# Optimization experiments

Measured on AMD Instinct MI355X. Metric: run time of the kernel, lower is better.

Reference implementation:

```python
import jax, jax.numpy as jnp
import numpy as np

B, P, N, E, H, D = 64, 256, 1000, 128, 8, 16
SQRT_E = 11.313708498984761  # sqrt(embedding_dim)
CLIP = 10.0                  # logit_clipping


def setup_inputs() -> dict:
    key = jax.random.key(0)
    ks = jax.random.split(key, 9)
    s = 0.05  # weight init scale
    return {
        "encoded_nodes": jax.random.normal(ks[0], (B, N, E), jnp.float32),
        "encoded_last_node": jax.random.normal(ks[1], (B, P, E), jnp.float32),
        "attr": jax.random.uniform(ks[2], (B, P, 1), jnp.float32),
        "ninf_mask": jnp.zeros((B, P, N), jnp.float32),
        # params stored [in, out] (apply as x @ W, equals torch Linear with W.T)
        "Wq_last": jax.random.normal(ks[3], (E + 1, H * D), jnp.float32) * s,
        "Wk": jax.random.normal(ks[4], (E, H * D), jnp.float32) * s,
        "Wv": jax.random.normal(ks[5], (E, H * D), jnp.float32) * s,
        "Wo": jax.random.normal(ks[6], (H * D, E), jnp.float32) * s,
        "bo": jax.random.normal(ks[7], (E,), jnp.float32) * s,
    }


def reference(encoded_nodes, encoded_last_node, attr, ninf_mask,
              Wq_last, Wk, Wv, Wo, bo):
    # set_kv: project encoded nodes to per-head K, V  -> [B, N, H, D]
    k = (encoded_nodes @ Wk).reshape(B, N, H, D)
    v = (encoded_nodes @ Wv).reshape(B, N, H, D)

    # query from (last node embedding, attr) -> [B, P, H, D]
    input_cat = jnp.concatenate([encoded_last_node, attr], axis=2)  # [B,P,E+1]
    q = (input_cat @ Wq_last).reshape(B, P, H, D)

    # multi-head attention with additive rank-3 -inf mask
    inv_sqrt_d = 1.0 / jnp.sqrt(jnp.float32(D))
    scores = jnp.einsum("bphd,bnhd->bhpn", q, k) * inv_sqrt_d
    scores = scores + ninf_mask[:, None, :, :]            # [B,H,P,N]
    weights = jax.nn.softmax(scores, axis=-1)
    out = jnp.einsum("bhpn,bnhd->bphd", weights, v).reshape(B, P, H * D)

    mh = out @ Wo + bo                                    # [B,P,E]

    # single-head tanh-clipped scoring against encoded nodes
    score = jnp.einsum("bpe,bne->bpn", mh, encoded_nodes) / SQRT_E
    score_masked = CLIP * jnp.tanh(score) + ninf_mask
    probs = jax.nn.softmax(score_masked, axis=2)          # [B,P,N]
    return probs
```

## Files before the change

### kernel.cpp

```cpp
#include <hip/hip_runtime.h>

#define BB 64
#define PP 256
#define NN 1000
#define NP 1024
#define EE 128
#define HH 8
#define DD 16

typedef __fp16 v4h __attribute__((ext_vector_type(4)));
typedef float v4f __attribute__((ext_vector_type(4)));


__global__ __launch_bounds__(256) void k1_qproj(const float* __restrict__ ln,
                                                const float* __restrict__ attr,
                                                const float* __restrict__ Wq,
                                                __fp16* __restrict__ Qh) {
    __shared__ __fp16 wt[128 * 132];
    __shared__ float attrs[64];
    const int tid = threadIdx.x;
    const int row0 = blockIdx.x * 64;
    for (int i = tid; i < 128 * 128; i += 256) {
        int k = i >> 7, n = i & 127;
        wt[n * 132 + k] = (__fp16)Wq[i];
    }
    if (tid < 64) attrs[tid] = attr[row0 + tid];
    __syncthreads();

    const int wid = tid >> 6, lane = tid & 63;
    const int lp = lane & 15, lg = lane >> 4;
    const int rb = row0 + wid * 16;

    const float* arow = ln + (size_t)(rb + lp) * 128;
    v4f acc[8];
#pragma unroll
    for (int cf = 0; cf < 8; cf++) acc[cf] = (v4f){0.f, 0.f, 0.f, 0.f};

#pragma unroll
    for (int k0 = 0; k0 < 8; k0++) {
        float4 av = *(const float4*)&arow[k0 * 16 + 4 * lg];
        v4h af;
        af[0] = (__fp16)av.x; af[1] = (__fp16)av.y;
        af[2] = (__fp16)av.z; af[3] = (__fp16)av.w;
#pragma unroll
        for (int cf = 0; cf < 8; cf++) {
            v4h bf = *(const v4h*)&wt[(cf * 16 + lp) * 132 + k0 * 16 + 4 * lg];
            acc[cf] = __builtin_amdgcn_mfma_f32_16x16x16f16(af, bf, acc[cf], 0, 0, 0);
        }
    }

#pragma unroll
    for (int cf = 0; cf < 8; cf++) {
        const int col = cf * 16 + lp;
        const float w128 = Wq[128 * 128 + col];
#pragma unroll
        for (int r = 0; r < 4; r++) {
            const int rl = wid * 16 + 4 * lg + r;
            float v = (acc[cf][r] + attrs[rl] * w128) * 0.25f;
            Qh[(size_t)(row0 + rl) * 128 + col] = (__fp16)v;
        }
    }
}

__global__ __launch_bounds__(256) void k2_kv(const float* __restrict__ nodes,
                                             const float* __restrict__ Wk,
                                             const float* __restrict__ Wv,
                                             __fp16* __restrict__ Kf,
                                             __fp16* __restrict__ Vf) {
    __shared__ __fp16 wt[128 * 132];
    const int tid = threadIdx.x;
    const int b = blockIdx.y;
    const int kv = blockIdx.z;
    const float* W = (kv == 0) ? Wk : Wv;
    for (int i = tid; i < 128 * 128; i += 256) {
        int k = i >> 7, n = i & 127;
        wt[n * 132 + k] = (__fp16)W[i];
    }
    __syncthreads();

    const int wid = tid >> 6, lane = tid & 63;
    const int lp = lane & 15, lg = lane >> 4;
    const int nb = blockIdx.x * 64 + wid * 16;

    int nr = nb + lp;
    if (nr >= NN) nr = NN - 1;
    const float* arow = nodes + (size_t)(b * NN + nr) * 128;

    v4f acc[8];
#pragma unroll
    for (int cf = 0; cf < 8; cf++) acc[cf] = (v4f){0.f, 0.f, 0.f, 0.f};

#pragma unroll
    for (int k0 = 0; k0 < 8; k0++) {
        float4 av = *(const float4*)&arow[k0 * 16 + 4 * lg];
        v4h af;
        af[0] = (__fp16)av.x; af[1] = (__fp16)av.y;
        af[2] = (__fp16)av.z; af[3] = (__fp16)av.w;
#pragma unroll
        for (int cf = 0; cf < 8; cf++) {
            v4h bf = *(const v4h*)&wt[(cf * 16 + lp) * 132 + k0 * 16 + 4 * lg];
            acc[cf] = __builtin_amdgcn_mfma_f32_16x16x16f16(af, bf, acc[cf], 0, 0, 0);
        }
    }

    if (kv == 0) {
#pragma unroll
        for (int cf = 0; cf < 8; cf++) {
            const size_t base = ((size_t)(b * HH + cf) << 14) + lp;
#pragma unroll
            for (int r = 0; r < 4; r++) {
                const int n = nb + 4 * lg + r;
                Kf[base + (size_t)n * 16] = (n < NN) ? (__fp16)acc[cf][r] : (__fp16)0.f;
            }
        }
    } else {
#pragma unroll
        for (int cf = 0; cf < 8; cf++) {
            v4h pk;
#pragma unroll
            for (int r = 0; r < 4; r++) {
                const int n = nb + 4 * lg + r;
                pk[r] = (n < NN) ? (__fp16)acc[cf][r] : (__fp16)0.f;
            }
            *(v4h*)&Vf[(((size_t)(b * HH + cf) * 16 + lp) << 10) + nb + 4 * lg] = pk;
        }
    }
}

__global__ __launch_bounds__(256) void k3_attn(const __fp16* __restrict__ Qh,
                                               const __fp16* __restrict__ Kf,
                                               const __fp16* __restrict__ Vf,
                                               const float* __restrict__ mask,
                                               float* __restrict__ Aout) {
    const int tid = threadIdx.x;
    const int bid = blockIdx.x;
    const int b = bid & 63;
    const int c = bid >> 6;
    const int hg = c & 3, pt = c >> 2;
    const int h0 = hg * 2;
    const int p0 = pt * 64;

    const int wid = tid >> 6, lane = tid & 63;
    const int lp = lane & 15, lg = lane >> 4;
    const int pw = p0 + wid * 16;

    v4h qf[2];
    {
        const __fp16* qrow = Qh + (size_t)(b * PP + pw + lp) * 128 + h0 * 16 + 4 * lg;
#pragma unroll
        for (int j = 0; j < 2; j++) qf[j] = *(const v4h*)&qrow[j * 16];
    }

    v4f acc[2];
    float lsum[2];
#pragma unroll
    for (int j = 0; j < 2; j++) { acc[j] = (v4f){0.f, 0.f, 0.f, 0.f}; lsum[j] = 0.f; }
    const v4f zero4 = {0.f, 0.f, 0.f, 0.f};

    const __fp16* kp = Kf + ((size_t)(b * HH + h0) << 14);
    const __fp16* vp = Vf + ((size_t)((b * HH + h0) * 16) << 10);
    const float* mrow = mask + (size_t)(b * PP + pw + lp) * NN;

#pragma unroll 2
    for (int s = 0; s < 62; s++) {
        const int nl = s * 16;
        v4h kf[2], vf[2];
#pragma unroll
        for (int j = 0; j < 2; j++)
            kf[j] = *(const v4h*)&kp[(j << 14) + (nl + lp) * 16 + 4 * lg];
#pragma unroll
        for (int j = 0; j < 2; j++)
            vf[j] = *(const v4h*)&vp[(j << 14) + lp * NP + nl + 4 * lg];
        float4 mv = *(const float4*)&mrow[nl + 4 * lg];
#pragma unroll
        for (int j = 0; j < 2; j++) {
            v4f sc = __builtin_amdgcn_mfma_f32_16x16x16f16(kf[j], qf[j], zero4, 0, 0, 0);
            float w0 = __expf(sc[0] + mv.x);
            float w1 = __expf(sc[1] + mv.y);
            float w2 = __expf(sc[2] + mv.z);
            float w3 = __expf(sc[3] + mv.w);
            lsum[j] += (w0 + w1) + (w2 + w3);
            v4h wf;
            wf[0] = (__fp16)w0; wf[1] = (__fp16)w1; wf[2] = (__fp16)w2; wf[3] = (__fp16)w3;
            acc[j] = __builtin_amdgcn_mfma_f32_16x16x16f16(wf, vf[j], acc[j], 0, 0, 0);
        }
    }
    {
        const int nl = 992;
        int nc = nl + 4 * lg; if (nc > 996) nc = 996;
        float4 mv = *(const float4*)&mrow[nc];
        const bool b0 = (nl + 4 * lg + 0 < NN), b1 = (nl + 4 * lg + 1 < NN);
        const bool b2 = (nl + 4 * lg + 2 < NN), b3 = (nl + 4 * lg + 3 < NN);
#pragma unroll
        for (int j = 0; j < 2; j++) {
            v4h kf = *(const v4h*)&kp[(j << 14) + (nl + lp) * 16 + 4 * lg];
            v4h vf = *(const v4h*)&vp[(j << 14) + lp * NP + nl + 4 * lg];
            v4f sc = __builtin_amdgcn_mfma_f32_16x16x16f16(kf, qf[j], zero4, 0, 0, 0);
            float w0 = b0 ? __expf(sc[0] + mv.x) : 0.f;
            float w1 = b1 ? __expf(sc[1] + mv.y) : 0.f;
            float w2 = b2 ? __expf(sc[2] + mv.z) : 0.f;
            float w3 = b3 ? __expf(sc[3] + mv.w) : 0.f;
            lsum[j] += (w0 + w1) + (w2 + w3);
            v4h wf;
            wf[0] = (__fp16)w0; wf[1] = (__fp16)w1; wf[2] = (__fp16)w2; wf[3] = (__fp16)w3;
            acc[j] = __builtin_amdgcn_mfma_f32_16x16x16f16(wf, vf, acc[j], 0, 0, 0);
        }
    }

#pragma unroll
    for (int j = 0; j < 2; j++) {
        float l = lsum[j];
        l += __shfl_xor(l, 16);
        l += __shfl_xor(l, 32);
#pragma unroll
        for (int r = 0; r < 4; r++) {
            float denom = __shfl(l, 4 * lg + r);
            float inv = 1.f / denom;
            Aout[(size_t)(b * PP + pw + 4 * lg + r) * 128 + (h0 + j) * 16 + lp] =
                acc[j][r] * inv;
        }
    }
}

__global__ __launch_bounds__(256) void k4_mh(const float* __restrict__ Ain,
                                             const float* __restrict__ Wo,
                                             const float* __restrict__ bo,
                                             __fp16* __restrict__ Mh) {
    __shared__ __fp16 wt[128 * 132];
    const int tid = threadIdx.x;
    const int row0 = blockIdx.x * 64;
    for (int i = tid; i < 128 * 128; i += 256) {
        int k = i >> 7, n = i & 127;
        wt[n * 132 + k] = (__fp16)Wo[i];
    }
    __syncthreads();

    const int wid = tid >> 6, lane = tid & 63;
    const int lp = lane & 15, lg = lane >> 4;
    const int rb = row0 + wid * 16;

    const float* arow = Ain + (size_t)(rb + lp) * 128;
    v4f acc[8];
#pragma unroll
    for (int cf = 0; cf < 8; cf++) acc[cf] = (v4f){0.f, 0.f, 0.f, 0.f};

#pragma unroll
    for (int k0 = 0; k0 < 8; k0++) {
        float4 av = *(const float4*)&arow[k0 * 16 + 4 * lg];
        v4h af;
        af[0] = (__fp16)av.x; af[1] = (__fp16)av.y;
        af[2] = (__fp16)av.z; af[3] = (__fp16)av.w;
#pragma unroll
        for (int cf = 0; cf < 8; cf++) {
            v4h bf = *(const v4h*)&wt[(cf * 16 + lp) * 132 + k0 * 16 + 4 * lg];
            acc[cf] = __builtin_amdgcn_mfma_f32_16x16x16f16(af, bf, acc[cf], 0, 0, 0);
        }
    }

    const float scale = 0.08838834764831845f;
#pragma unroll
    for (int cf = 0; cf < 8; cf++) {
        const int col = cf * 16 + lp;
        const float bb = bo[col];
#pragma unroll
        for (int r = 0; r < 4; r++) {
            const int rl = wid * 16 + 4 * lg + r;
            Mh[(size_t)(row0 + rl) * 128 + col] = (__fp16)((acc[cf][r] + bb) * scale);
        }
    }
}

__global__ __launch_bounds__(256) void k5_final(const float* __restrict__ nodes,
                                                const __fp16* __restrict__ Mh,
                                                const float* __restrict__ mask,
                                                float* __restrict__ out) {
    __shared__ __fp16 probs[16 * 1028];
    __shared__ float rowsum[16];
    __shared__ float rowinv[16];
    const int tid = threadIdx.x;
    const int bid = blockIdx.x;
    const int xcd = bid & 7;
    const int rest = bid >> 3;
    const int pt = rest & 15;
    const int b = ((rest >> 4) << 3) + xcd;
    const int p0 = pt * 16;

    if (tid < 16) rowsum[tid] = 0.f;

    const int wid = tid >> 6, lane = tid & 63;
    const int lp = lane & 15, lg = lane >> 4;

    v4h bf[8];
    {
        const __fp16* mhrow = Mh + (size_t)(b * PP + p0 + lp) * 128;
#pragma unroll
        for (int ec = 0; ec < 8; ec++)
            bf[ec] = *(const v4h*)&mhrow[ec * 16 + 4 * lg];
    }
    __syncthreads();

    float lsum = 0.f;
    const float* nbase = nodes + (size_t)b * NN * 128;
    const float* mkrow = mask + (size_t)(b * PP + p0 + lp) * NN;
    const v4f zero4 = {0.f, 0.f, 0.f, 0.f};

    for (int s = 0; s < 16; s++) {
        const int nt = s * 64 + wid * 16;
        int nr = nt + lp;
        if (nr >= NN) nr = NN - 1;
        const float* arow = nbase + (size_t)nr * 128;
        v4f acc = zero4;
#pragma unroll
        for (int ec = 0; ec < 8; ec++) {
            float4 av = *(const float4*)&arow[ec * 16 + 4 * lg];
            v4h af;
            af[0] = (__fp16)av.x; af[1] = (__fp16)av.y;
            af[2] = (__fp16)av.z; af[3] = (__fp16)av.w;
            acc = __builtin_amdgcn_mfma_f32_16x16x16f16(af, bf[ec], acc, 0, 0, 0);
        }
        const int nb4 = nt + 4 * lg;
        v4h wf;
        if (nt + 15 < NN) {
            float4 mkv = *(const float4*)&mkrow[nb4];
            float e0 = __expf(2.f * acc[0]);
            float e1 = __expf(2.f * acc[1]);
            float e2 = __expf(2.f * acc[2]);
            float e3 = __expf(2.f * acc[3]);
            float w0 = __expf(fmaf(-20.f, __builtin_amdgcn_rcpf(e0 + 1.f), mkv.x));
            float w1 = __expf(fmaf(-20.f, __builtin_amdgcn_rcpf(e1 + 1.f), mkv.y));
            float w2 = __expf(fmaf(-20.f, __builtin_amdgcn_rcpf(e2 + 1.f), mkv.z));
            float w3 = __expf(fmaf(-20.f, __builtin_amdgcn_rcpf(e3 + 1.f), mkv.w));
            lsum += (w0 + w1) + (w2 + w3);
            wf[0] = (__fp16)w0; wf[1] = (__fp16)w1; wf[2] = (__fp16)w2; wf[3] = (__fp16)w3;
        } else {
            float w[4];
#pragma unroll
            for (int r = 0; r < 4; r++) {
                if (nb4 + r < NN) {
                    float e = __expf(2.f * acc[r]);
                    w[r] = __expf(fmaf(-20.f, __builtin_amdgcn_rcpf(e + 1.f),
                                       mkrow[nb4 + r]));
                } else {
                    w[r] = 0.f;
                }
            }
            lsum += (w[0] + w[1]) + (w[2] + w[3]);
            wf[0] = (__fp16)w[0]; wf[1] = (__fp16)w[1];
            wf[2] = (__fp16)w[2]; wf[3] = (__fp16)w[3];
        }
        *(v4h*)&probs[lp * 1028 + nb4] = wf;
    }

    lsum += __shfl_xor(lsum, 16);
    lsum += __shfl_xor(lsum, 32);
    if (lane < 16) atomicAdd(&rowsum[lane], lsum);
    __syncthreads();
    if (tid < 16) rowinv[tid] = 1.f / rowsum[tid];
    __syncthreads();

    if (tid < 250) {
        const int c4 = tid * 4;
        const size_t obase = (size_t)(b * PP + p0) * NN;
#pragma unroll 4
        for (int r = 0; r < 16; r++) {
            v4h pv = *(const v4h*)&probs[r * 1028 + c4];
            float inv = rowinv[r];
            float4 ov;
            ov.x = (float)pv[0] * inv;
            ov.y = (float)pv[1] * inv;
            ov.z = (float)pv[2] * inv;
            ov.w = (float)pv[3] * inv;
            *(float4*)&out[obase + (size_t)r * NN + c4] = ov;
        }
    }
}

extern "C" void kernel_launch(void* const* d_in, const int* in_sizes, int n_in,
                              void* d_out, int out_size, void* d_ws, size_t ws_size,
                              hipStream_t stream) {
    const float* nodes = (const float*)d_in[0];
    const float* ln    = (const float*)d_in[1];
    const float* attr  = (const float*)d_in[2];
    const float* mask  = (const float*)d_in[3];
    const float* Wq    = (const float*)d_in[4];
    const float* Wk    = (const float*)d_in[5];
    const float* Wv    = (const float*)d_in[6];
    const float* Wo    = (const float*)d_in[7];
    const float* bo    = (const float*)d_in[8];
    float* out = (float*)d_out;

    float*  Aout = (float*)d_ws;
    __fp16* Qh   = (__fp16*)(Aout + 2097152);
    __fp16* Mhh  = Qh + 2097152;

    __fp16* Kf = (__fp16*)d_out;
    __fp16* Vf = Kf + (size_t)BB * HH * NP * 16;

    hipLaunchKernelGGL(k1_qproj, dim3(256), dim3(256), 0, stream, ln, attr, Wq, Qh);
    hipLaunchKernelGGL(k2_kv, dim3(16, 64, 2), dim3(256), 0, stream, nodes, Wk, Wv, Kf, Vf);
    hipLaunchKernelGGL(k3_attn, dim3(1024), dim3(256), 0, stream, Qh, Kf, Vf, mask, Aout);
    hipLaunchKernelGGL(k4_mh, dim3(256), dim3(256), 0, stream, Aout, Wo, bo, Mhh);
    hipLaunchKernelGGL(k5_final, dim3(1024), dim3(256), 0, stream, nodes, Mhh, mask, out);
}
```

Before: 338.7 us.

## Stage K/V tiles through double-buffered shared memory in attention kernel

The V projection output is re-laid out into 16x16 tiles, so each 16-node K and V chunk per head is contiguous. Each of the four waves in a block loads one K or V tile per step into a double-buffered shared-memory array, with a register prefetch two steps ahead and the mask prefetched one step ahead. All waves then read fragments from LDS instead of each wave loading K and V from global memory separately. This removes redundant global loads across the four waves, at the cost of a block-wide barrier on every iteration.

```diff
diff --git a/kernel.cpp b/kernel.cpp
--- a/kernel.cpp
+++ b/kernel.cpp
@@ -66,7 +66,7 @@
                                              const float* __restrict__ Wk,
                                              const float* __restrict__ Wv,
                                              __fp16* __restrict__ Kf,
-                                             __fp16* __restrict__ Vf) {
+                                             __fp16* __restrict__ Vt) {
     __shared__ __fp16 wt[128 * 132];
     const int tid = threadIdx.x;
     const int b = blockIdx.y;
@@ -122,21 +122,23 @@
                 const int n = nb + 4 * lg + r;
                 pk[r] = (n < NN) ? (__fp16)acc[cf][r] : (__fp16)0.f;
             }
-            *(v4h*)&Vf[(((size_t)(b * HH + cf) * 16 + lp) << 10) + nb + 4 * lg] = pk;
+            *(v4h*)&Vt[((size_t)(b * HH + cf) << 14) + (size_t)(nb >> 4) * 256 +
+                       lp * 16 + 4 * lg] = pk;
         }
     }
 }
 
 __global__ __launch_bounds__(256) void k3_attn(const __fp16* __restrict__ Qh,
                                                const __fp16* __restrict__ Kf,
-                                               const __fp16* __restrict__ Vf,
+                                               const __fp16* __restrict__ Vt,
                                                const float* __restrict__ mask,
                                                float* __restrict__ Aout) {
+    __shared__ __fp16 sh[2][4][256];
     const int tid = threadIdx.x;
     const int bid = blockIdx.x;
     const int b = bid & 63;
-    const int c = bid >> 6;
-    const int hg = c & 3, pt = c >> 2;
+    const int rest = bid >> 6;
+    const int hg = rest & 3, pt = rest >> 2;
     const int h0 = hg * 2;
     const int p0 = pt * 64;
 
@@ -144,66 +146,108 @@
     const int lp = lane & 15, lg = lane >> 4;
     const int pw = p0 + wid * 16;
 
+    const __fp16* gsrc = ((wid < 2) ? Kf + ((size_t)(b * HH + h0 + wid) << 14)
+                                    : Vt + ((size_t)(b * HH + h0 + wid - 2) << 14)) +
+                         lane * 4;
+    __fp16* sdst0 = &sh[0][wid][lane * 4];
+    __fp16* sdst1 = &sh[1][wid][lane * 4];
+
     v4h qf[2];
     {
         const __fp16* qrow = Qh + (size_t)(b * PP + pw + lp) * 128 + h0 * 16 + 4 * lg;
-#pragma unroll
-        for (int j = 0; j < 2; j++) qf[j] = *(const v4h*)&qrow[j * 16];
-    }
+        qf[0] = *(const v4h*)&qrow[0];
+        qf[1] = *(const v4h*)&qrow[16];
+    }
+
+    const float* mrow = mask + (size_t)(b * PP + pw + lp) * NN;
 
     v4f acc[2];
     float lsum[2];
-#pragma unroll
-    for (int j = 0; j < 2; j++) { acc[j] = (v4f){0.f, 0.f, 0.f, 0.f}; lsum[j] = 0.f; }
+    acc[0] = (v4f){0.f, 0.f, 0.f, 0.f};
+    acc[1] = (v4f){0.f, 0.f, 0.f, 0.f};
+    lsum[0] = 0.f; lsum[1] = 0.f;
     const v4f zero4 = {0.f, 0.f, 0.f, 0.f};
 
-    const __fp16* kp = Kf + ((size_t)(b * HH + h0) << 14);
-    const __fp16* vp = Vf + ((size_t)((b * HH + h0) * 16) << 10);
-    const float* mrow = mask + (size_t)(b * PP + pw + lp) * NN;
+    v4h st[2];
+    float4 mv[2];
+    st[0] = *(const v4h*)(gsrc);
+    *(v4h*)sdst0 = st[0];
+    st[1] = *(const v4h*)(gsrc + 256);
+    mv[0] = *(const float4*)&mrow[4 * lg];
+    __syncthreads();
 
 #pragma unroll 2
     for (int s = 0; s < 62; s++) {
-        const int nl = s * 16;
-        v4h kf[2], vf[2];
-#pragma unroll
-        for (int j = 0; j < 2; j++)
-            kf[j] = *(const v4h*)&kp[(j << 14) + (nl + lp) * 16 + 4 * lg];
-#pragma unroll
-        for (int j = 0; j < 2; j++)
-            vf[j] = *(const v4h*)&vp[(j << 14) + lp * NP + nl + 4 * lg];
-        float4 mv = *(const float4*)&mrow[nl + 4 * lg];
-#pragma unroll
-        for (int j = 0; j < 2; j++) {
-            v4f sc = __builtin_amdgcn_mfma_f32_16x16x16f16(kf[j], qf[j], zero4, 0, 0, 0);
-            float w0 = __expf(sc[0] + mv.x);
-            float w1 = __expf(sc[1] + mv.y);
-            float w2 = __expf(sc[2] + mv.z);
-            float w3 = __expf(sc[3] + mv.w);
-            lsum[j] += (w0 + w1) + (w2 + w3);
+        const int p = s & 1;
+        if (s + 2 <= 62) st[p] = *(const v4h*)(gsrc + (s + 2) * 256);
+        {
+            int moff = (s + 1) * 16 + 4 * lg;
+            if (moff > 996) moff = 996;
+            mv[p ^ 1] = *(const float4*)&mrow[moff];
+        }
+
+        v4h kf0 = *(const v4h*)&sh[p][0][lp * 16 + 4 * lg];
+        v4h kf1 = *(const v4h*)&sh[p][1][lp * 16 + 4 * lg];
+        v4h vf0 = *(const v4h*)&sh[p][2][lp * 16 + 4 * lg];
+        v4h vf1 = *(const v4h*)&sh[p][3][lp * 16 + 4 * lg];
+        const float4 m = mv[p];
+        {
+            v4f sc = __builtin_amdgcn_mfma_f32_16x16x16f16(kf0, qf[0], zero4, 0, 0, 0);
+            float w0 = __expf(sc[0] + m.x);
+            float w1 = __expf(sc[1] + m.y);
+            float w2 = __expf(sc[2] + m.z);
+            float w3 = __expf(sc[3] + m.w);
+            lsum[0] += (w0 + w1) + (w2 + w3);
             v4h wf;
             wf[0] = (__fp16)w0; wf[1] = (__fp16)w1; wf[2] = (__fp16)w2; wf[3] = (__fp16)w3;
-            acc[j] = __builtin_amdgcn_mfma_f32_16x16x16f16(wf, vf[j], acc[j], 0, 0, 0);
-        }
-    }
+            acc[0] = __builtin_amdgcn_mfma_f32_16x16x16f16(wf, vf0, acc[0], 0, 0, 0);
+        }
+        {
+            v4f sc = __builtin_amdgcn_mfma_f32_16x16x16f16(kf1, qf[1], zero4, 0, 0, 0);
+            float w0 = __expf(sc[0] + m.x);
+            float w1 = __expf(sc[1] + m.y);
+            float w2 = __expf(sc[2] + m.z);
+            float w3 = __expf(sc[3] + m.w);
+            lsum[1] += (w0 + w1) + (w2 + w3);
+            v4h wf;
+            wf[0] = (__fp16)w0; wf[1] = (__fp16)w1; wf[2] = (__fp16)w2; wf[3] = (__fp16)w3;
+            acc[1] = __builtin_amdgcn_mfma_f32_16x16x16f16(wf, vf1, acc[1], 0, 0, 0);
+        }
+
+        *(v4h*)((p == 0) ? sdst1 : sdst0) = st[p ^ 1];
+        __syncthreads();
+    }
+
     {
         const int nl = 992;
-        int nc = nl + 4 * lg; if (nc > 996) nc = 996;
-        float4 mv = *(const float4*)&mrow[nc];
-        const bool b0 = (nl + 4 * lg + 0 < NN), b1 = (nl + 4 * lg + 1 < NN);
-        const bool b2 = (nl + 4 * lg + 2 < NN), b3 = (nl + 4 * lg + 3 < NN);
-#pragma unroll
-        for (int j = 0; j < 2; j++) {
-            v4h kf = *(const v4h*)&kp[(j << 14) + (nl + lp) * 16 + 4 * lg];
-            v4h vf = *(const v4h*)&vp[(j << 14) + lp * NP + nl + 4 * lg];
-            v4f sc = __builtin_amdgcn_mfma_f32_16x16x16f16(kf, qf[j], zero4, 0, 0, 0);
-            float w0 = b0 ? __expf(sc[0] + mv.x) : 0.f;
-            float w1 = b1 ? __expf(sc[1] + mv.y) : 0.f;
-            float w2 = b2 ? __expf(sc[2] + mv.z) : 0.f;
-            float w3 = b3 ? __expf(sc[3] + mv.w) : 0.f;
-            lsum[j] += (w0 + w1) + (w2 + w3);
+        const float4 m = mv[0];
+        const bool c0 = (nl + 4 * lg + 0 < NN), c1 = (nl + 4 * lg + 1 < NN);
+        const bool c2 = (nl + 4 * lg + 2 < NN), c3 = (nl + 4 * lg + 3 < NN);
+        v4h kf0 = *(const v4h*)&sh[0][0][lp * 16 + 4 * lg];
+        v4h kf1 = *(const v4h*)&sh[0][1][lp * 16 + 4 * lg];
+        v4h vf0 = *(const v4h*)&sh[0][2][lp * 16 + 4 * lg];
+        v4h vf1 = *(const v4h*)&sh[0][3][lp * 16 + 4 * lg];
+        {
+            v4f sc = __builtin_amdgcn_mfma_f32_16x16x16f16(kf0, qf[0], zero4, 0, 0, 0);
+            float w0 = c0 ? __expf(sc[0] + m.x) : 0.f;
+            float w1 = c1 ? __expf(sc[1] + m.y) : 0.f;
+            float w2 = c2 ? __expf(sc[2] + m.z) : 0.f;
+            float w3 = c3 ? __expf(sc[3] + m.w) : 0.f;
+            lsum[0] += (w0 + w1) + (w2 + w3);
             v4h wf;
             wf[0] = (__fp16)w0; wf[1] = (__fp16)w1; wf[2] = (__fp16)w2; wf[3] = (__fp16)w3;
-            acc[j] = __builtin_amdgcn_mfma_f32_16x16x16f16(wf, vf, acc[j], 0, 0, 0);
+            acc[0] = __builtin_amdgcn_mfma_f32_16x16x16f16(wf, vf0, acc[0], 0, 0, 0);
+        }
+        {
+            v4f sc = __builtin_amdgcn_mfma_f32_16x16x16f16(kf1, qf[1], zero4, 0, 0, 0);
+            float w0 = c0 ? __expf(sc[0] + m.x) : 0.f;
+            float w1 = c1 ? __expf(sc[1] + m.y) : 0.f;
+            float w2 = c2 ? __expf(sc[2] + m.z) : 0.f;
+            float w3 = c3 ? __expf(sc[3] + m.w) : 0.f;
+            lsum[1] += (w0 + w1) + (w2 + w3);
+            v4h wf;
+            wf[0] = (__fp16)w0; wf[1] = (__fp16)w1; wf[2] = (__fp16)w2; wf[3] = (__fp16)w3;
+            acc[1] = __builtin_amdgcn_mfma_f32_16x16x16f16(wf, vf1, acc[1], 0, 0, 0);
         }
     }
 
@@ -394,11 +438,11 @@
     __fp16* Mhh  = Qh + 2097152;
 
     __fp16* Kf = (__fp16*)d_out;
-    __fp16* Vf = Kf + (size_t)BB * HH * NP * 16;
+    __fp16* Vt = Kf + (size_t)BB * HH * NP * 16;
 
     hipLaunchKernelGGL(k1_qproj, dim3(256), dim3(256), 0, stream, ln, attr, Wq, Qh);
-    hipLaunchKernelGGL(k2_kv, dim3(16, 64, 2), dim3(256), 0, stream, nodes, Wk, Wv, Kf, Vf);
-    hipLaunchKernelGGL(k3_attn, dim3(1024), dim3(256), 0, stream, Qh, Kf, Vf, mask, Aout);
+    hipLaunchKernelGGL(k2_kv, dim3(16, 64, 2), dim3(256), 0, stream, nodes, Wk, Wv, Kf, Vt);
+    hipLaunchKernelGGL(k3_attn, dim3(1024), dim3(256), 0, stream, Qh, Kf, Vt, mask, Aout);
     hipLaunchKernelGGL(k4_mh, dim3(256), dim3(256), 0, stream, Aout, Wo, bo, Mhh);
     hipLaunchKernelGGL(k5_final, dim3(1024), dim3(256), 0, stream, nodes, Mhh, mask, out);
 }
```

Result: faster. 302.1 us (-10.8%).
